# Performance work log

Hardware: AMD Instinct MI355X
Metric: run time of the kernel (lower is better)

## Reference

```python
import jax, jax.numpy as jnp
import numpy as np

B, H, W = 8, 64, 64
C = 256
NUM_HEADS = 8
HEAD_DIM = C // NUM_HEADS  # 32
K0, K1 = 7, 13  # two neighborhood kernel sizes (dilation = 1)


def _starts(L, K):
    """NATTEN (dilation=1) window start and relative-bias start per position."""
    nh = K // 2
    i = jnp.arange(L)
    win = jnp.maximum(i - nh, 0) + jnp.where(i + nh >= L, L - i - nh - 1, 0)
    pb = nh + jnp.where(i < nh, nh - i, 0) + jnp.where(i + nh >= L, L - i - 1 - nh, 0)
    return win, pb


def _na2d(q, k, v, rpb, K):
    """2D neighborhood attention with relative positional bias.
    q,k,v: [B,h,H,W,D] (q pre-scaled); rpb: [h, 2K-1, 2K-1]."""
    Bq, h, Hq, Wq, D = q.shape
    sh, ph = _starts(Hq, K)
    sw, pw = _starts(Wq, K)
    kk = jnp.arange(K)
    idx_h = sh[:, None] + kk            # [H,K] neighbor row indices
    idx_w = sw[:, None] + kk            # [W,K] neighbor col indices
    rows = ph[:, None] + kk             # [H,K] rpb row offsets
    cols = pw[:, None] + kk             # [W,K] rpb col offsets
    # bias[hd,i,ki,j,kj] = rpb[hd, rows[i,ki], cols[j,kj]] -> [h,H,K,W,K]
    bias = rpb[:, rows[:, :, None, None], cols[None, None, :, :]]
    bias = bias.transpose(0, 1, 3, 2, 4)  # [h,H,W,K,K]
    # QK: loop over the K kernel rows (small fixed set) to avoid a [B,h,H,K,W,K,D] blowup
    attn_rows = []
    for ki in range(K):
        kh = jnp.take(k, idx_h[:, ki], axis=2)      # [B,h,H,W,D]
        khw = jnp.take(kh, idx_w, axis=3)           # [B,h,H,W,K,D]
        attn_rows.append(jnp.einsum('bhijd,bhijkd->bhijk', q, khw))
    attn = jnp.stack(attn_rows, axis=4)             # [B,h,H,W,K,K]
    attn = attn + bias[None]
    attn = jax.nn.softmax(attn.reshape(Bq, h, Hq, Wq, K * K), axis=-1)
    attn = attn.reshape(Bq, h, Hq, Wq, K, K)
    # AV: same row-wise gather
    out = jnp.zeros_like(q)
    for ki in range(K):
        vh = jnp.take(v, idx_h[:, ki], axis=2)      # [B,h,H,W,D]
        vhw = jnp.take(vh, idx_w, axis=3)           # [B,h,H,W,K,D]
        out = out + jnp.einsum('bhijk,bhijkd->bhijd', attn[:, :, :, :, ki, :], vhw)
    return out


def setup_inputs() -> dict:
    key = jax.random.key(0)
    ks = jax.random.split(key, 7)
    x = jax.random.normal(ks[0], (B, H, W, C), dtype=jnp.float32)
    w_qkv = jax.random.normal(ks[1], (3 * C, C), dtype=jnp.float32) * 0.02
    b_qkv = jnp.zeros((3 * C,), dtype=jnp.float32)
    rpb0 = jnp.clip(jax.random.normal(ks[2], (NUM_HEADS // 2, 2 * K0 - 1, 2 * K0 - 1), dtype=jnp.float32) * 0.02, -2.0, 2.0)
    rpb1 = jnp.clip(jax.random.normal(ks[3], (NUM_HEADS // 2, 2 * K1 - 1, 2 * K1 - 1), dtype=jnp.float32) * 0.02, -2.0, 2.0)
    w_proj = jax.random.normal(ks[4], (C, C), dtype=jnp.float32) * 0.02
    b_proj = jnp.zeros((C,), dtype=jnp.float32)
    return {"x": x, "w_qkv": w_qkv, "b_qkv": b_qkv, "rpb0": rpb0, "rpb1": rpb1,
            "w_proj": w_proj, "b_proj": b_proj}


def reference(x, w_qkv, b_qkv, rpb0, rpb1, w_proj, b_proj):
    Bx, Hx, Wx, Cx = x.shape
    nh, hd = NUM_HEADS, Cx // NUM_HEADS
    qkv = (x @ w_qkv.T + b_qkv).reshape(Bx, Hx, Wx, 3, nh, hd)
    qkv = qkv.transpose(3, 0, 4, 1, 2, 5)           # [3,B,nh,H,W,hd]
    q, k, v = qkv[0], qkv[1], qkv[2]
    q = q * (hd ** -0.5)
    half = nh // 2
    x0 = _na2d(q[:, :half], k[:, :half], v[:, :half], rpb0, K0)
    x1 = _na2d(q[:, half:], k[:, half:], v[:, half:], rpb1, K1)
    y = jnp.concatenate([x0, x1], axis=1)           # [B,nh,H,W,hd]
    y = y.transpose(0, 2, 3, 1, 4).reshape(Bx, Hx, Wx, Cx)
    return y @ w_proj.T + b_proj
```

## Files before the change

### kernel.cpp

```cpp
#include <hip/hip_runtime.h>
#include <hip/hip_bf16.h>

typedef __attribute__((ext_vector_type(8))) short short8;
typedef __attribute__((ext_vector_type(4))) float f32x4;

#define GM 32768
#define DH 32
#define LOG2E 1.4426950408889634f

__device__ __forceinline__ ushort f2bf(float f) {
  unsigned int u = __float_as_uint(f);
  u += 0x7FFFu + ((u >> 16) & 1u);
  return (ushort)(u >> 16);
}
__device__ __forceinline__ unsigned int cvtpk(float a, float b) {
  unsigned int r;
  asm("v_cvt_pk_bf16_f32 %0, %1, %2" : "=v"(r) : "v"(a), "v"(b));
  return r;
}

template<int MODE>
__global__ __launch_bounds__(256) void gemm_bt(
    const float* __restrict__ Af, const ushort* __restrict__ Ab,
    const float* __restrict__ Bf,
    ushort* __restrict__ Cb, ushort* __restrict__ Vt,
    float* __restrict__ Cf, const float* __restrict__ bias, float scale) {
  const int BM = 128, BN = 128, BK = 64, K = 256;
  __shared__ int4 sAB[2 * BM * BK / 8];
  int4* sA4 = sAB;
  int4* sB4 = sAB + BM * BK / 8;

  int id = blockIdx.x;
  int xcd = id & 7, rest = id >> 3;
  int bm, bn;
  if (MODE == 0) { bm = xcd * 32 + rest / 6;    bn = rest % 6; }
  else           { bm = xcd * 32 + (rest >> 1); bn = rest & 1; }

  int tid = threadIdx.x;
  int lane = tid & 63, wid = tid >> 6;
  int wm = (wid >> 1) * 64, wn = (wid & 1) * 64;
  int lo = lane & 15, hi = lane >> 4;

  f32x4 acc[4][4] = {};

  for (int kt = 0; kt < K; kt += BK) {
    int4 ra[4], rb[4];
#pragma unroll
    for (int i = 0; i < 4; ++i) {
      int cid = tid + i * 256;
      int r = cid >> 3, c = cid & 7;
      if (MODE == 0) {
        const float* p = Af + (size_t)(bm * BM + r) * K + kt + c * 8;
        float4 t0 = *(const float4*)p, t1 = *(const float4*)(p + 4);
        ra[i] = make_int4(cvtpk(t0.x, t0.y), cvtpk(t0.z, t0.w),
                          cvtpk(t1.x, t1.y), cvtpk(t1.z, t1.w));
      } else {
        ra[i] = *(const int4*)(Ab + (size_t)(bm * BM + r) * K + kt + c * 8);
      }
      const float* q = Bf + (size_t)(bn * BN + r) * K + kt + c * 8;
      float4 s0 = *(const float4*)q, s1 = *(const float4*)(q + 4);
      rb[i] = make_int4(cvtpk(s0.x, s0.y), cvtpk(s0.z, s0.w),
                        cvtpk(s1.x, s1.y), cvtpk(s1.z, s1.w));
    }
    __syncthreads();
#pragma unroll
    for (int i = 0; i < 4; ++i) {
      int cid = tid + i * 256;
      int r = cid >> 3, c = cid & 7;
      sA4[r * 8 + (c ^ (r & 7))] = ra[i];
      sB4[r * 8 + (c ^ (r & 7))] = rb[i];
    }
    __syncthreads();
#pragma unroll
    for (int ks = 0; ks < 2; ++ks) {
      short8 af[4], bfr[4];
#pragma unroll
      for (int mi = 0; mi < 4; ++mi) {
        int r = wm + mi * 16 + lo, c = ks * 4 + hi;
        af[mi] = ((const short8*)sA4)[r * 8 + (c ^ (r & 7))];
      }
#pragma unroll
      for (int nj = 0; nj < 4; ++nj) {
        int r = wn + nj * 16 + lo, c = ks * 4 + hi;
        bfr[nj] = ((const short8*)sB4)[r * 8 + (c ^ (r & 7))];
      }
#pragma unroll
      for (int mi = 0; mi < 4; ++mi)
#pragma unroll
        for (int nj = 0; nj < 4; ++nj)
          acc[mi][nj] = __builtin_amdgcn_mfma_f32_16x16x32_bf16(
              af[mi], bfr[nj], acc[mi][nj], 0, 0, 0);
    }
  }

  if (MODE == 0) {
    float sc = (bn < 2) ? scale : 1.0f;
    __syncthreads();
    ushort* sC = (ushort*)sAB;
#pragma unroll
    for (int mi = 0; mi < 4; ++mi)
#pragma unroll
      for (int nj = 0; nj < 4; ++nj)
#pragma unroll
        for (int r = 0; r < 4; ++r) {
          int row = wm + mi * 16 + hi * 4 + r;
          int col = wn + nj * 16 + lo;
          float v = (acc[mi][nj][r] + bias[bn * BN + col]) * sc;
          sC[row * 128 + (((col >> 3) ^ (row & 15)) << 3) + (col & 7)] = f2bf(v);
        }
    __syncthreads();
    if (bn < 4) {
      int sel = bn >> 1;
      size_t base0 = ((size_t)(sel * 8 + (bn & 1) * 4) * GM + (size_t)bm * BM) * DH;
#pragma unroll
      for (int p8 = 0; p8 < 8; ++p8) {
        int o = p8 * 256 + tid;
        int hh = o >> 9, row = (o >> 2) & 127, q = o & 3;
        int4 val = *(const int4*)(sC + row * 128 + (((hh * 4 + q) ^ (row & 15)) << 3));
        *(int4*)(Cb + base0 + (size_t)hh * GM * DH + row * DH + q * 8) = val;
      }
    } else {
      int hb32 = (bn - 4) * 128;
#pragma unroll
      for (int p8 = 0; p8 < 8; ++p8) {
        int o = p8 * 256 + tid;
        int col = o >> 4, chunk = o & 15;
        int4 val;
        ushort* vp = (ushort*)&val;
#pragma unroll
        for (int e = 0; e < 8; ++e) {
          int row = chunk * 8 + e;
          vp[e] = sC[row * 128 + (((col >> 3) ^ (row & 15)) << 3) + (col & 7)];
        }
        *(int4*)(Vt + (size_t)(hb32 + col) * GM + (size_t)bm * BM + chunk * 8) = val;
      }
    }
  } else {
#pragma unroll
    for (int mi = 0; mi < 4; ++mi)
#pragma unroll
      for (int nj = 0; nj < 4; ++nj)
#pragma unroll
        for (int r = 0; r < 4; ++r) {
          int row = bm * BM + wm + mi * 16 + hi * 4 + r;
          int col = bn * BN + wn + nj * 16 + lo;
          Cf[(size_t)row * 256 + col] = acc[mi][nj][r] + bias[col];
        }
  }
}

template<int KS>
__device__ __forceinline__ void natt_pair(const ushort* __restrict__ qkvb,
                                          const ushort* __restrict__ vt,
                                          const float* __restrict__ rpb,
                                          ushort* __restrict__ y,
                                          float* sbias, unsigned int* sP,
                                          int b, int hl, int h, int i0) {
  const int NHF = KS / 2, BW = 2 * KS - 1, LK = 64 - KS, TS = KS * BW;
  int tid = threadIdx.x;
  int lane = tid & 63, w = tid >> 6, lo = lane & 15, hi = lane >> 4;
  int i1 = i0 + 1;

  int wi0 = i0 - NHF; wi0 = wi0 < 0 ? 0 : (wi0 > LK ? LK : wi0);
  int wi1 = i1 - NHF; wi1 = wi1 < 0 ? 0 : (wi1 > LK ? LK : wi1);
  int d = wi1 - wi0;
  int pi0 = NHF + ((i0 < NHF) ? (NHF - i0) : 0) + ((i0 >= 64 - NHF) ? (63 - NHF - i0) : 0);
  int pi1 = NHF + ((i1 < NHF) ? (NHF - i1) : 0) + ((i1 >= 64 - NHF) ? (63 - NHF - i1) : 0);

  for (int t = tid; t < 4 * TS; t += 256) {
    float v = -1e30f;
    if (t < TS) {
      int ki = t / BW, cb = t - ki * BW;
      v = rpb[((size_t)hl * BW + pi0 + ki) * BW + cb] * LOG2E;
    } else if (t < 2 * TS) {
      int tt = t - TS, ki = tt / BW, cb = tt - ki * BW;
      v = rpb[((size_t)hl * BW + pi1 + ki) * BW + cb] * LOG2E;
    }
    sbias[t] = v;
  }
  __syncthreads();

  const ushort* qb = qkvb;
  const ushort* kb = qkvb + (size_t)8 * GM * DH;

  int jbase = 16 * w;
  int j = jbase + lo;
  size_t posQ0 = (size_t)h * GM + b * 4096 + i0 * 64 + j;
  short8 aq0 = *(const short8*)(qb + posQ0 * DH + hi * 8);
  short8 aq1 = *(const short8*)(qb + (posQ0 + 64) * DH + hi * 8);

  int wj16 = jbase - NHF; wj16 = wj16 < 0 ? 0 : (wj16 > LK ? LK : wj16);
  int cbase = wj16 < 32 ? wj16 : 32;
  int wj = j - NHF; wj = wj < 0 ? 0 : (wj > LK ? LK : wj);

  int aoff[8];
#pragma unroll
  for (int t = 0; t < 8; ++t) {
    int c = cbase + (t >> 2) * 16 + hi * 4 + (t & 3);
    int idx = c - j + (KS - 1);
    bool valid = (c >= wj) && (c < wj + KS);
    aoff[t] = valid ? idx * 4 : 2 * TS * 4;
  }
  int rbase1 = (TS - d * BW) * 4;

  unsigned int* base0 = sP + (w * 4) * 320;
  unsigned int* base1 = sP + (w * 4 + 2) * 320;
  int pwo1 = lo * 20 + 2 * hi, pwo2 = lo * 20 + 8 + 2 * hi, pro = lo * 20 + 4 * hi;

  const char* sb = (const char*)sbias;
  const ushort* kband = kb + ((size_t)h * GM + b * 4096 + (size_t)wi0 * 64 + cbase) * DH;
  const ushort* vrow0 = vt + ((size_t)h * DH + lo) * GM
                        + ((size_t)b * 4096 + (size_t)wi0 * 64 + cbase + hi * 8);
  const ushort* vrow1 = vrow0 + (size_t)16 * GM;

#define LOADK(KI, F0, F1) { const ushort* kr_ = kband + (KI) * 64 * DH; \
    F0 = *(const short8*)(kr_ + lo * DH + hi * 8); \
    F1 = *(const short8*)(kr_ + (16 + lo) * DH + hi * 8); }
#define LOADV(KI, F0, F1) { \
    F0 = *(const short8*)(vrow0 + (KI) * 64); \
    F1 = *(const short8*)(vrow1 + (KI) * 64); }

  const f32x4 zero = {};
  f32x4 o0_0 = {}, o1_0 = {}, o0_1 = {}, o1_1 = {};
  float dena0 = 0.f, denb0 = 0.f, dena1 = 0.f, denb1 = 0.f;

  short8 ck0, ck1, cv0, cv1, nk0, nk1, nv0, nv1, vp0, vp1;
  LOADK(0, ck0, ck1);
  LOADV(0, cv0, cv1);
  nk0 = ck0; nk1 = ck1; nv0 = cv0; nv1 = cv1;
  vp0 = cv0; vp1 = cv1;

  int tend = KS + d;
  for (int t = 0; t <= tend; ++t) {
    if (t + 1 < tend) { LOADK(t + 1, nk0, nk1); LOADV(t + 1, nv0, nv1); }
    int slot = (t & 1) * 320, slotp = ((t - 1) & 1) * 320;
    int tb = t * BW * 4;
    if (t < KS) {
      f32x4 s0 = __builtin_amdgcn_mfma_f32_16x16x32_bf16(ck0, aq0, zero, 0, 0, 0);
      f32x4 s1 = __builtin_amdgcn_mfma_f32_16x16x32_bf16(ck1, aq0, zero, 0, 0, 0);
      float p[8];
#pragma unroll
      for (int e = 0; e < 8; ++e) {
        float bv = *(const float*)(sb + (aoff[e] + tb));
        float sv = (e < 4) ? s0[e & 3] : s1[e & 3];
        float ex;
        asm("v_exp_f32 %0, %1" : "=v"(ex) : "v"(sv + bv));
        p[e] = ex;
        if (e & 1) denb0 += ex; else dena0 += ex;
      }
      *(uint2*)(base0 + slot + pwo1) = make_uint2(cvtpk(p[0], p[1]), cvtpk(p[2], p[3]));
      *(uint2*)(base0 + slot + pwo2) = make_uint2(cvtpk(p[4], p[5]), cvtpk(p[6], p[7]));
    }
    if (t >= d && t < KS + d) {
      f32x4 s0 = __builtin_amdgcn_mfma_f32_16x16x32_bf16(ck0, aq1, zero, 0, 0, 0);
      f32x4 s1 = __builtin_amdgcn_mfma_f32_16x16x32_bf16(ck1, aq1, zero, 0, 0, 0);
      float p[8];
#pragma unroll
      for (int e = 0; e < 8; ++e) {
        float bv = *(const float*)(sb + (aoff[e] + rbase1 + tb));
        float sv = (e < 4) ? s0[e & 3] : s1[e & 3];
        float ex;
        asm("v_exp_f32 %0, %1" : "=v"(ex) : "v"(sv + bv));
        p[e] = ex;
        if (e & 1) denb1 += ex; else dena1 += ex;
      }
      *(uint2*)(base1 + slot + pwo1) = make_uint2(cvtpk(p[0], p[1]), cvtpk(p[2], p[3]));
      *(uint2*)(base1 + slot + pwo2) = make_uint2(cvtpk(p[4], p[5]), cvtpk(p[6], p[7]));
    }
    if (t >= 1 && t <= KS) {
      short8 pa = *(const short8*)(base0 + slotp + pro);
      o0_0 = __builtin_amdgcn_mfma_f32_16x16x32_bf16(pa, vp0, o0_0, 0, 0, 0);
      o1_0 = __builtin_amdgcn_mfma_f32_16x16x32_bf16(pa, vp1, o1_0, 0, 0, 0);
    }
    if (t >= d + 1) {
      short8 pa = *(const short8*)(base1 + slotp + pro);
      o0_1 = __builtin_amdgcn_mfma_f32_16x16x32_bf16(pa, vp0, o0_1, 0, 0, 0);
      o1_1 = __builtin_amdgcn_mfma_f32_16x16x32_bf16(pa, vp1, o1_1, 0, 0, 0);
    }
    vp0 = cv0; vp1 = cv1;
    cv0 = nv0; cv1 = nv1;
    ck0 = nk0; ck1 = nk1;
  }
#undef LOADK
#undef LOADV

#pragma unroll
  for (int r = 0; r < 2; ++r) {
    float den = (r == 0) ? (dena0 + denb0) : (dena1 + denb1);
    den += __shfl_xor(den, 16);
    den += __shfl_xor(den, 32);
    float inv = 1.f / den;
    float dinv[4];
#pragma unroll
    for (int q = 0; q < 4; ++q) dinv[q] = __shfl(inv, hi * 4 + q);
    f32x4 oa = (r == 0) ? o0_0 : o0_1;
    f32x4 ob = (r == 0) ? o1_0 : o1_1;
    size_t ybase = ((size_t)b * 4096 + (size_t)(i0 + r) * 64 + jbase) * 256 + h * DH;
#pragma unroll
    for (int q = 0; q < 4; ++q) {
      int jr = hi * 4 + q;
      y[ybase + (size_t)jr * 256 + lo]      = f2bf(oa[q] * dinv[q]);
      y[ybase + (size_t)jr * 256 + 16 + lo] = f2bf(ob[q] * dinv[q]);
    }
  }
}

__global__ __launch_bounds__(256) void natt_mfma(const ushort* __restrict__ qkvb,
    const ushort* __restrict__ vt, const float* __restrict__ rpb0,
    const float* __restrict__ rpb1, ushort* __restrict__ y) {
  __shared__ float sbias[4 * 13 * 25];
  __shared__ unsigned int sP[4 * 4 * 320];
  int blk = blockIdx.x;
  int xcd = blk & 7, rest = blk >> 3;
  int b = rest >> 5, i0 = (rest & 31) * 2;
  int ho = (xcd - b) & 7;
  if (ho < 4) natt_pair<13>(qkvb, vt, rpb1, y, sbias, sP, b, ho, ho + 4, i0);
  else        natt_pair<7> (qkvb, vt, rpb0, y, sbias, sP, b, ho - 4, ho - 4, i0);
}

extern "C" void kernel_launch(void* const* d_in, const int* in_sizes, int n_in,
                              void* d_out, int out_size, void* d_ws, size_t ws_size,
                              hipStream_t stream) {
  const float* x      = (const float*)d_in[0];
  const float* w_qkv  = (const float*)d_in[1];
  const float* b_qkv  = (const float*)d_in[2];
  const float* rpb0   = (const float*)d_in[3];
  const float* rpb1   = (const float*)d_in[4];
  const float* w_proj = (const float*)d_in[5];
  const float* b_proj = (const float*)d_in[6];
  float* out = (float*)d_out;

  char* ws = (char*)d_ws;
  ushort* qkvb = (ushort*)(ws);
  ushort* vt   = (ushort*)(ws + (32u << 20));
  ushort* yb   = (ushort*)(ws + (48u << 20));

  gemm_bt<0><<<1536, 256, 0, stream>>>(x, nullptr, w_qkv, qkvb, vt, nullptr, b_qkv,
                                       0.17677669529663687f * LOG2E);
  natt_mfma<<<2048, 256, 0, stream>>>(qkvb, vt, rpb0, rpb1, yb);
  gemm_bt<1><<<512, 256, 0, stream>>>(nullptr, yb, w_proj, nullptr, nullptr, out,
                                      b_proj, 1.0f);
}
```

Measured before the change: 198.4 us.

## Pre-cast weights to bf16, prefetch GEMM tiles, process four rows per attention block

A small kernel now converts both weight matrices to bf16 once per call, so the GEMMs load bf16 B tiles instead of converting fp32 in every block. The GEMM main loop prefetches the next K tile into registers while MFMAs run on the current one. The V-transpose epilogue writes a transposed shared tile so each thread stores with one vector read instead of eight scalar reads. The attention kernel handles four query rows per block instead of two, sharing each K/V band load across more rows and halving the grid. The cost is higher register and LDS use, which may lower occupancy.

```diff
diff --git a/kernel.cpp b/kernel.cpp
--- a/kernel.cpp
+++ b/kernel.cpp
@@ -19,58 +19,71 @@
   return r;
 }
 
+__global__ __launch_bounds__(256) void cast_w(const float* __restrict__ wq,
+                                              const float* __restrict__ wp,
+                                              ushort* __restrict__ wqb,
+                                              ushort* __restrict__ wpb) {
+  int idx = (blockIdx.x * 256 + threadIdx.x) * 4;
+  const float* src; ushort* dst; int k;
+  if (idx < 196608) { src = wq; dst = wqb; k = idx; }
+  else              { src = wp; dst = wpb; k = idx - 196608; }
+  float4 t = *(const float4*)(src + k);
+  ushort4 o;
+  o.x = f2bf(t.x); o.y = f2bf(t.y); o.z = f2bf(t.z); o.w = f2bf(t.w);
+  *(ushort4*)(dst + k) = o;
+}
+
 template<int MODE>
 __global__ __launch_bounds__(256) void gemm_bt(
     const float* __restrict__ Af, const ushort* __restrict__ Ab,
-    const float* __restrict__ Bf,
+    const ushort* __restrict__ Btb,
     ushort* __restrict__ Cb, ushort* __restrict__ Vt,
     float* __restrict__ Cf, const float* __restrict__ bias, float scale) {
   const int BM = 128, BN = 128, BK = 64, K = 256;
-  __shared__ int4 sAB[2 * BM * BK / 8];
+  __shared__ int4 sAB[2048];
   int4* sA4 = sAB;
-  int4* sB4 = sAB + BM * BK / 8;
-
-  int id = blockIdx.x;
-  int xcd = id & 7, rest = id >> 3;
+  int4* sB4 = sAB + 1024;
+
+  int id = blockIdx.x, xcd = id & 7, rest = id >> 3;
   int bm, bn;
   if (MODE == 0) { bm = xcd * 32 + rest / 6;    bn = rest % 6; }
   else           { bm = xcd * 32 + (rest >> 1); bn = rest & 1; }
 
-  int tid = threadIdx.x;
-  int lane = tid & 63, wid = tid >> 6;
+  int tid = threadIdx.x, lane = tid & 63, wid = tid >> 6;
   int wm = (wid >> 1) * 64, wn = (wid & 1) * 64;
   int lo = lane & 15, hi = lane >> 4;
 
   f32x4 acc[4][4] = {};
-
-  for (int kt = 0; kt < K; kt += BK) {
-    int4 ra[4], rb[4];
-#pragma unroll
-    for (int i = 0; i < 4; ++i) {
-      int cid = tid + i * 256;
-      int r = cid >> 3, c = cid & 7;
-      if (MODE == 0) {
-        const float* p = Af + (size_t)(bm * BM + r) * K + kt + c * 8;
-        float4 t0 = *(const float4*)p, t1 = *(const float4*)(p + 4);
-        ra[i] = make_int4(cvtpk(t0.x, t0.y), cvtpk(t0.z, t0.w),
-                          cvtpk(t1.x, t1.y), cvtpk(t1.z, t1.w));
-      } else {
-        ra[i] = *(const int4*)(Ab + (size_t)(bm * BM + r) * K + kt + c * 8);
-      }
-      const float* q = Bf + (size_t)(bn * BN + r) * K + kt + c * 8;
-      float4 s0 = *(const float4*)q, s1 = *(const float4*)(q + 4);
-      rb[i] = make_int4(cvtpk(s0.x, s0.y), cvtpk(s0.z, s0.w),
-                        cvtpk(s1.x, s1.y), cvtpk(s1.z, s1.w));
+  float4 raf[8], raf2[8];
+  int4 rai[4], rai2[4], rbi[4], rbi2[4];
+
+#define GLOADA(KT, RAF, RAI) { _Pragma("unroll") \
+  for (int ii = 0; ii < 4; ++ii) { int cid = tid + ii * 256, rr = cid >> 3, cc = cid & 7; \
+    if (MODE == 0) { const float* p = Af + (size_t)(bm * BM + rr) * K + (KT) * BK + cc * 8; \
+      RAF[2*ii] = *(const float4*)p; RAF[2*ii+1] = *(const float4*)(p + 4); } \
+    else RAI[ii] = *(const int4*)(Ab + (size_t)(bm * BM + rr) * K + (KT) * BK + cc * 8); } }
+#define GLOADB(KT, RBI) { _Pragma("unroll") \
+  for (int ii = 0; ii < 4; ++ii) { int cid = tid + ii * 256, rr = cid >> 3, cc = cid & 7; \
+    RBI[ii] = *(const int4*)(Btb + (size_t)(bn * BN + rr) * K + (KT) * BK + cc * 8); } }
+
+  GLOADA(0, raf, rai);
+  GLOADB(0, rbi);
+
+#pragma unroll
+  for (int kt = 0; kt < 4; ++kt) {
+#pragma unroll
+    for (int ii = 0; ii < 4; ++ii) {
+      int cid = tid + ii * 256, rr = cid >> 3, cc = cid & 7;
+      int4 av;
+      if (MODE == 0)
+        av = make_int4(cvtpk(raf[2*ii].x, raf[2*ii].y), cvtpk(raf[2*ii].z, raf[2*ii].w),
+                       cvtpk(raf[2*ii+1].x, raf[2*ii+1].y), cvtpk(raf[2*ii+1].z, raf[2*ii+1].w));
+      else av = rai[ii];
+      sA4[rr * 8 + (cc ^ (rr & 7))] = av;
+      sB4[rr * 8 + (cc ^ (rr & 7))] = rbi[ii];
     }
     __syncthreads();
-#pragma unroll
-    for (int i = 0; i < 4; ++i) {
-      int cid = tid + i * 256;
-      int r = cid >> 3, c = cid & 7;
-      sA4[r * 8 + (c ^ (r & 7))] = ra[i];
-      sB4[r * 8 + (c ^ (r & 7))] = rb[i];
-    }
-    __syncthreads();
+    if (kt < 3) { GLOADA(kt + 1, raf2, rai2); GLOADB(kt + 1, rbi2); }
 #pragma unroll
     for (int ks = 0; ks < 2; ++ks) {
       short8 af[4], bfr[4];
@@ -91,25 +104,34 @@
           acc[mi][nj] = __builtin_amdgcn_mfma_f32_16x16x32_bf16(
               af[mi], bfr[nj], acc[mi][nj], 0, 0, 0);
     }
-  }
+    __syncthreads();
+    if (kt < 3) {
+#pragma unroll
+      for (int ii = 0; ii < 4; ++ii) {
+        rai[ii] = rai2[ii]; rbi[ii] = rbi2[ii];
+        raf[2*ii] = raf2[2*ii]; raf[2*ii+1] = raf2[2*ii+1];
+      }
+    }
+  }
+#undef GLOADA
+#undef GLOADB
 
   if (MODE == 0) {
     float sc = (bn < 2) ? scale : 1.0f;
-    __syncthreads();
     ushort* sC = (ushort*)sAB;
-#pragma unroll
-    for (int mi = 0; mi < 4; ++mi)
-#pragma unroll
-      for (int nj = 0; nj < 4; ++nj)
-#pragma unroll
-        for (int r = 0; r < 4; ++r) {
-          int row = wm + mi * 16 + hi * 4 + r;
-          int col = wn + nj * 16 + lo;
-          float v = (acc[mi][nj][r] + bias[bn * BN + col]) * sc;
-          sC[row * 128 + (((col >> 3) ^ (row & 15)) << 3) + (col & 7)] = f2bf(v);
-        }
-    __syncthreads();
     if (bn < 4) {
+#pragma unroll
+      for (int mi = 0; mi < 4; ++mi)
+#pragma unroll
+        for (int nj = 0; nj < 4; ++nj)
+#pragma unroll
+          for (int r = 0; r < 4; ++r) {
+            int row = wm + mi * 16 + hi * 4 + r;
+            int col = wn + nj * 16 + lo;
+            float v = (acc[mi][nj][r] + bias[bn * BN + col]) * sc;
+            sC[row * 128 + (((col >> 3) ^ (row & 15)) << 3) + (col & 7)] = f2bf(v);
+          }
+      __syncthreads();
       int sel = bn >> 1;
       size_t base0 = ((size_t)(sel * 8 + (bn & 1) * 4) * GM + (size_t)bm * BM) * DH;
 #pragma unroll
@@ -120,19 +142,24 @@
         *(int4*)(Cb + base0 + (size_t)hh * GM * DH + row * DH + q * 8) = val;
       }
     } else {
+#pragma unroll
+      for (int mi = 0; mi < 4; ++mi)
+#pragma unroll
+        for (int nj = 0; nj < 4; ++nj)
+#pragma unroll
+          for (int r = 0; r < 4; ++r) {
+            int row = wm + mi * 16 + hi * 4 + r;
+            int col = wn + nj * 16 + lo;
+            float v = acc[mi][nj][r] + bias[bn * BN + col];
+            sC[col * 128 + (((row >> 3) ^ (col & 15)) << 3) + (row & 7)] = f2bf(v);
+          }
+      __syncthreads();
       int hb32 = (bn - 4) * 128;
 #pragma unroll
       for (int p8 = 0; p8 < 8; ++p8) {
-        int o = p8 * 256 + tid;
-        int col = o >> 4, chunk = o & 15;
-        int4 val;
-        ushort* vp = (ushort*)&val;
-#pragma unroll
-        for (int e = 0; e < 8; ++e) {
-          int row = chunk * 8 + e;
-          vp[e] = sC[row * 128 + (((col >> 3) ^ (row & 15)) << 3) + (col & 7)];
-        }
-        *(int4*)(Vt + (size_t)(hb32 + col) * GM + (size_t)bm * BM + chunk * 8) = val;
+        int chunk = tid & 15, colg = p8 * 16 + (tid >> 4);
+        int4 val = *(const int4*)(sC + colg * 128 + ((chunk ^ (colg & 15)) << 3));
+        *(int4*)(Vt + (size_t)(hb32 + colg) * GM + (size_t)bm * BM + chunk * 8) = val;
       }
     }
   } else {
@@ -150,7 +177,7 @@
 }
 
 template<int KS>
-__device__ __forceinline__ void natt_pair(const ushort* __restrict__ qkvb,
+__device__ __forceinline__ void natt_quad(const ushort* __restrict__ qkvb,
                                           const ushort* __restrict__ vt,
                                           const float* __restrict__ rpb,
                                           ushort* __restrict__ y,
@@ -159,22 +186,30 @@
   const int NHF = KS / 2, BW = 2 * KS - 1, LK = 64 - KS, TS = KS * BW;
   int tid = threadIdx.x;
   int lane = tid & 63, w = tid >> 6, lo = lane & 15, hi = lane >> 4;
-  int i1 = i0 + 1;
-
-  int wi0 = i0 - NHF; wi0 = wi0 < 0 ? 0 : (wi0 > LK ? LK : wi0);
-  int wi1 = i1 - NHF; wi1 = wi1 < 0 ? 0 : (wi1 > LK ? LK : wi1);
-  int d = wi1 - wi0;
-  int pi0 = NHF + ((i0 < NHF) ? (NHF - i0) : 0) + ((i0 >= 64 - NHF) ? (63 - NHF - i0) : 0);
-  int pi1 = NHF + ((i1 < NHF) ? (NHF - i1) : 0) + ((i1 >= 64 - NHF) ? (63 - NHF - i1) : 0);
-
-  for (int t = tid; t < 4 * TS; t += 256) {
+
+  int wi_[4], d_[4], rb_[4];
+#pragma unroll
+  for (int r = 0; r < 4; ++r) {
+    int i = i0 + r;
+    int wi = i - NHF; wi = wi < 0 ? 0 : (wi > LK ? LK : wi);
+    wi_[r] = wi;
+  }
+  int wi0 = wi_[0];
+#pragma unroll
+  for (int r = 0; r < 4; ++r) {
+    d_[r] = wi_[r] - wi0;
+    rb_[r] = (r * TS - d_[r] * BW) * 4;
+  }
+  int d3 = d_[3];
+
+  for (int t = tid; t < 8 * TS + 2 * BW; t += 256) {
     float v = -1e30f;
-    if (t < TS) {
-      int ki = t / BW, cb = t - ki * BW;
-      v = rpb[((size_t)hl * BW + pi0 + ki) * BW + cb] * LOG2E;
-    } else if (t < 2 * TS) {
-      int tt = t - TS, ki = tt / BW, cb = tt - ki * BW;
-      v = rpb[((size_t)hl * BW + pi1 + ki) * BW + cb] * LOG2E;
+    if (t < 4 * TS) {
+      int r = t / TS, tt = t - r * TS;
+      int ki = tt / BW, cb = tt - ki * BW;
+      int i = i0 + r;
+      int pi = NHF + ((i < NHF) ? (NHF - i) : 0) + ((i >= 64 - NHF) ? (63 - NHF - i) : 0);
+      v = rpb[((size_t)hl * BW + pi + ki) * BW + cb] * LOG2E;
     }
     sbias[t] = v;
   }
@@ -185,9 +220,11 @@
 
   int jbase = 16 * w;
   int j = jbase + lo;
-  size_t posQ0 = (size_t)h * GM + b * 4096 + i0 * 64 + j;
-  short8 aq0 = *(const short8*)(qb + posQ0 * DH + hi * 8);
-  short8 aq1 = *(const short8*)(qb + (posQ0 + 64) * DH + hi * 8);
+  size_t posQ = (size_t)h * GM + b * 4096 + i0 * 64 + j;
+  short8 aq0 = *(const short8*)(qb + posQ * DH + hi * 8);
+  short8 aq1 = *(const short8*)(qb + (posQ + 64) * DH + hi * 8);
+  short8 aq2 = *(const short8*)(qb + (posQ + 128) * DH + hi * 8);
+  short8 aq3 = *(const short8*)(qb + (posQ + 192) * DH + hi * 8);
 
   int wj16 = jbase - NHF; wj16 = wj16 < 0 ? 0 : (wj16 > LK ? LK : wj16);
   int cbase = wj16 < 32 ? wj16 : 32;
@@ -199,14 +236,10 @@
     int c = cbase + (t >> 2) * 16 + hi * 4 + (t & 3);
     int idx = c - j + (KS - 1);
     bool valid = (c >= wj) && (c < wj + KS);
-    aoff[t] = valid ? idx * 4 : 2 * TS * 4;
-  }
-  int rbase1 = (TS - d * BW) * 4;
-
-  unsigned int* base0 = sP + (w * 4) * 320;
-  unsigned int* base1 = sP + (w * 4 + 2) * 320;
+    aoff[t] = valid ? idx * 4 : 4 * TS * 4;
+  }
+
   int pwo1 = lo * 20 + 2 * hi, pwo2 = lo * 20 + 8 + 2 * hi, pro = lo * 20 + 4 * hi;
-
   const char* sb = (const char*)sbias;
   const ushort* kband = kb + ((size_t)h * GM + b * 4096 + (size_t)wi0 * 64 + cbase) * DH;
   const ushort* vrow0 = vt + ((size_t)h * DH + lo) * GM
@@ -222,7 +255,9 @@
 
   const f32x4 zero = {};
   f32x4 o0_0 = {}, o1_0 = {}, o0_1 = {}, o1_1 = {};
+  f32x4 o0_2 = {}, o1_2 = {}, o0_3 = {}, o1_3 = {};
   float dena0 = 0.f, denb0 = 0.f, dena1 = 0.f, denb1 = 0.f;
+  float dena2 = 0.f, denb2 = 0.f, dena3 = 0.f, denb3 = 0.f;
 
   short8 ck0, ck1, cv0, cv1, nk0, nk1, nv0, nv1, vp0, vp1;
   LOADK(0, ck0, ck1);
@@ -230,92 +265,82 @@
   nk0 = ck0; nk1 = ck1; nv0 = cv0; nv1 = cv1;
   vp0 = cv0; vp1 = cv1;
 
-  int tend = KS + d;
+#define ROWQK(R, AQ, DENA, DENB) \
+  if (t >= d_[R] && t < KS + d_[R]) { \
+    f32x4 s0 = __builtin_amdgcn_mfma_f32_16x16x32_bf16(ck0, AQ, zero, 0, 0, 0); \
+    f32x4 s1 = __builtin_amdgcn_mfma_f32_16x16x32_bf16(ck1, AQ, zero, 0, 0, 0); \
+    float p[8]; \
+    _Pragma("unroll") \
+    for (int e = 0; e < 8; ++e) { \
+      float bv = *(const float*)(sb + (aoff[e] + rb_[R] + tb)); \
+      float sv = (e < 4) ? s0[e & 3] : s1[e & 3]; \
+      float ex; asm("v_exp_f32 %0, %1" : "=v"(ex) : "v"(sv + bv)); \
+      p[e] = ex; if (e & 1) DENB += ex; else DENA += ex; \
+    } \
+    unsigned int* bp = sP + (w * 8 + R * 2) * 320 + slot; \
+    *(uint2*)(bp + pwo1) = make_uint2(cvtpk(p[0], p[1]), cvtpk(p[2], p[3])); \
+    *(uint2*)(bp + pwo2) = make_uint2(cvtpk(p[4], p[5]), cvtpk(p[6], p[7])); \
+  }
+#define ROWPV(R, O0, O1) \
+  if (t > d_[R] && t <= KS + d_[R]) { \
+    const unsigned int* bp = sP + (w * 8 + R * 2) * 320 + slotp; \
+    short8 pa = *(const short8*)(bp + pro); \
+    O0 = __builtin_amdgcn_mfma_f32_16x16x32_bf16(pa, vp0, O0, 0, 0, 0); \
+    O1 = __builtin_amdgcn_mfma_f32_16x16x32_bf16(pa, vp1, O1, 0, 0, 0); \
+  }
+
+  int tend = KS + d3;
   for (int t = 0; t <= tend; ++t) {
     if (t + 1 < tend) { LOADK(t + 1, nk0, nk1); LOADV(t + 1, nv0, nv1); }
     int slot = (t & 1) * 320, slotp = ((t - 1) & 1) * 320;
     int tb = t * BW * 4;
-    if (t < KS) {
-      f32x4 s0 = __builtin_amdgcn_mfma_f32_16x16x32_bf16(ck0, aq0, zero, 0, 0, 0);
-      f32x4 s1 = __builtin_amdgcn_mfma_f32_16x16x32_bf16(ck1, aq0, zero, 0, 0, 0);
-      float p[8];
-#pragma unroll
-      for (int e = 0; e < 8; ++e) {
-        float bv = *(const float*)(sb + (aoff[e] + tb));
-        float sv = (e < 4) ? s0[e & 3] : s1[e & 3];
-        float ex;
-        asm("v_exp_f32 %0, %1" : "=v"(ex) : "v"(sv + bv));
-        p[e] = ex;
-        if (e & 1) denb0 += ex; else dena0 += ex;
-      }
-      *(uint2*)(base0 + slot + pwo1) = make_uint2(cvtpk(p[0], p[1]), cvtpk(p[2], p[3]));
-      *(uint2*)(base0 + slot + pwo2) = make_uint2(cvtpk(p[4], p[5]), cvtpk(p[6], p[7]));
-    }
-    if (t >= d && t < KS + d) {
-      f32x4 s0 = __builtin_amdgcn_mfma_f32_16x16x32_bf16(ck0, aq1, zero, 0, 0, 0);
-      f32x4 s1 = __builtin_amdgcn_mfma_f32_16x16x32_bf16(ck1, aq1, zero, 0, 0, 0);
-      float p[8];
-#pragma unroll
-      for (int e = 0; e < 8; ++e) {
-        float bv = *(const float*)(sb + (aoff[e] + rbase1 + tb));
-        float sv = (e < 4) ? s0[e & 3] : s1[e & 3];
-        float ex;
-        asm("v_exp_f32 %0, %1" : "=v"(ex) : "v"(sv + bv));
-        p[e] = ex;
-        if (e & 1) denb1 += ex; else dena1 += ex;
-      }
-      *(uint2*)(base1 + slot + pwo1) = make_uint2(cvtpk(p[0], p[1]), cvtpk(p[2], p[3]));
-      *(uint2*)(base1 + slot + pwo2) = make_uint2(cvtpk(p[4], p[5]), cvtpk(p[6], p[7]));
-    }
-    if (t >= 1 && t <= KS) {
-      short8 pa = *(const short8*)(base0 + slotp + pro);
-      o0_0 = __builtin_amdgcn_mfma_f32_16x16x32_bf16(pa, vp0, o0_0, 0, 0, 0);
-      o1_0 = __builtin_amdgcn_mfma_f32_16x16x32_bf16(pa, vp1, o1_0, 0, 0, 0);
-    }
-    if (t >= d + 1) {
-      short8 pa = *(const short8*)(base1 + slotp + pro);
-      o0_1 = __builtin_amdgcn_mfma_f32_16x16x32_bf16(pa, vp0, o0_1, 0, 0, 0);
-      o1_1 = __builtin_amdgcn_mfma_f32_16x16x32_bf16(pa, vp1, o1_1, 0, 0, 0);
-    }
+    ROWQK(0, aq0, dena0, denb0)
+    ROWQK(1, aq1, dena1, denb1)
+    ROWQK(2, aq2, dena2, denb2)
+    ROWQK(3, aq3, dena3, denb3)
+    ROWPV(0, o0_0, o1_0)
+    ROWPV(1, o0_1, o1_1)
+    ROWPV(2, o0_2, o1_2)
+    ROWPV(3, o0_3, o1_3)
     vp0 = cv0; vp1 = cv1;
     cv0 = nv0; cv1 = nv1;
     ck0 = nk0; ck1 = nk1;
   }
 #undef LOADK
 #undef LOADV
-
-#pragma unroll
-  for (int r = 0; r < 2; ++r) {
-    float den = (r == 0) ? (dena0 + denb0) : (dena1 + denb1);
-    den += __shfl_xor(den, 16);
-    den += __shfl_xor(den, 32);
-    float inv = 1.f / den;
-    float dinv[4];
-#pragma unroll
-    for (int q = 0; q < 4; ++q) dinv[q] = __shfl(inv, hi * 4 + q);
-    f32x4 oa = (r == 0) ? o0_0 : o0_1;
-    f32x4 ob = (r == 0) ? o1_0 : o1_1;
-    size_t ybase = ((size_t)b * 4096 + (size_t)(i0 + r) * 64 + jbase) * 256 + h * DH;
-#pragma unroll
-    for (int q = 0; q < 4; ++q) {
-      int jr = hi * 4 + q;
-      y[ybase + (size_t)jr * 256 + lo]      = f2bf(oa[q] * dinv[q]);
-      y[ybase + (size_t)jr * 256 + 16 + lo] = f2bf(ob[q] * dinv[q]);
-    }
-  }
+#undef ROWQK
+#undef ROWPV
+
+#define ROWOUT(R, DENA, DENB, O0, O1) { \
+  float den = DENA + DENB; \
+  den += __shfl_xor(den, 16); den += __shfl_xor(den, 32); \
+  float inv = 1.f / den; \
+  size_t ybase = ((size_t)b * 4096 + (size_t)(i0 + R) * 64 + jbase) * 256 + h * DH; \
+  _Pragma("unroll") \
+  for (int q2 = 0; q2 < 4; ++q2) { \
+    float dv = __shfl(inv, hi * 4 + q2); \
+    y[ybase + (size_t)(hi * 4 + q2) * 256 + lo]      = f2bf(O0[q2] * dv); \
+    y[ybase + (size_t)(hi * 4 + q2) * 256 + 16 + lo] = f2bf(O1[q2] * dv); \
+  } }
+
+  ROWOUT(0, dena0, denb0, o0_0, o1_0)
+  ROWOUT(1, dena1, denb1, o0_1, o1_1)
+  ROWOUT(2, dena2, denb2, o0_2, o1_2)
+  ROWOUT(3, dena3, denb3, o0_3, o1_3)
+#undef ROWOUT
 }
 
 __global__ __launch_bounds__(256) void natt_mfma(const ushort* __restrict__ qkvb,
     const ushort* __restrict__ vt, const float* __restrict__ rpb0,
     const float* __restrict__ rpb1, ushort* __restrict__ y) {
-  __shared__ float sbias[4 * 13 * 25];
-  __shared__ unsigned int sP[4 * 4 * 320];
+  __shared__ float sbias[2656];
+  __shared__ unsigned int sP[10240];
   int blk = blockIdx.x;
   int xcd = blk & 7, rest = blk >> 3;
-  int b = rest >> 5, i0 = (rest & 31) * 2;
+  int b = rest >> 4, i0 = (rest & 15) * 4;
   int ho = (xcd - b) & 7;
-  if (ho < 4) natt_pair<13>(qkvb, vt, rpb1, y, sbias, sP, b, ho, ho + 4, i0);
-  else        natt_pair<7> (qkvb, vt, rpb0, y, sbias, sP, b, ho - 4, ho - 4, i0);
+  if (ho < 4) natt_quad<13>(qkvb, vt, rpb1, y, sbias, sP, b, ho, ho + 4, i0);
+  else        natt_quad<7> (qkvb, vt, rpb0, y, sbias, sP, b, ho - 4, ho - 4, i0);
 }
 
 extern "C" void kernel_launch(void* const* d_in, const int* in_sizes, int n_in,
@@ -334,10 +359,13 @@
   ushort* qkvb = (ushort*)(ws);
   ushort* vt   = (ushort*)(ws + (32u << 20));
   ushort* yb   = (ushort*)(ws + (48u << 20));
-
-  gemm_bt<0><<<1536, 256, 0, stream>>>(x, nullptr, w_qkv, qkvb, vt, nullptr, b_qkv,
+  ushort* wqb  = (ushort*)(ws + (64u << 20));
+  ushort* wpb  = (ushort*)(ws + (64u << 20) + 393216);
+
+  cast_w<<<256, 256, 0, stream>>>(w_qkv, w_proj, wqb, wpb);
+  gemm_bt<0><<<1536, 256, 0, stream>>>(x, nullptr, wqb, qkvb, vt, nullptr, b_qkv,
                                        0.17677669529663687f * LOG2E);
-  natt_mfma<<<2048, 256, 0, stream>>>(qkvb, vt, rpb0, rpb1, yb);
-  gemm_bt<1><<<512, 256, 0, stream>>>(nullptr, yb, w_proj, nullptr, nullptr, out,
+  natt_mfma<<<1024, 256, 0, stream>>>(qkvb, vt, rpb0, rpb1, yb);
+  gemm_bt<1><<<512, 256, 0, stream>>>(nullptr, yb, wpb, nullptr, nullptr, out,
                                       b_proj, 1.0f);
 }
```

Result: faster. 192.2 us (-3.1%).
